# Kernel tuning notes

Measured on AMD Instinct MI355X. Metric: run time of the kernel, lower is better.

The kernel has to match this reference:

```python
import jax, jax.numpy as jnp
import numpy as np

N_NODES = 50000
N_EDGES = 800000
NODE_IN = 5
EDGE_IN = 1
HID = 64


def setup_inputs() -> dict:
    key = jax.random.key(0)
    ks = jax.random.split(key, 16)
    x = jax.random.normal(ks[0], (N_NODES, NODE_IN), dtype=jnp.float32)
    edge_index = jax.random.randint(ks[1], (2, N_EDGES), 0, N_NODES, dtype=jnp.int32)
    edge_attr = jax.random.normal(ks[2], (N_EDGES, EDGE_IN), dtype=jnp.float32)
    def lin(k, fan_in, fan_out):
        b = 1.0 / np.sqrt(fan_in)
        k1, k2 = jax.random.split(k)
        W = jax.random.uniform(k1, (fan_in, fan_out), minval=-b, maxval=b, dtype=jnp.float32)
        bi = jax.random.uniform(k2, (fan_out,), minval=-b, maxval=b, dtype=jnp.float32)
        return W, bi
    W_ne, b_ne = lin(ks[3], NODE_IN, HID)
    W_ee, b_ee = lin(ks[4], EDGE_IN, HID)
    W_gcn, b_gcn = lin(ks[5], HID, HID)   # PyG GCNConv: lin (no bias) + separate bias
    W1, b1 = lin(ks[6], 3 * HID, HID)
    W2, b2 = lin(ks[7], HID, 1)
    return {"x": x, "edge_index": edge_index, "edge_attr": edge_attr,
            "W_ne": W_ne, "b_ne": b_ne, "W_ee": W_ee, "b_ee": b_ee,
            "W_gcn": W_gcn, "b_gcn": b_gcn, "W1": W1, "b1": b1, "W2": W2, "b2": b2}


def gcn_conv(h, edge_index, W, b):
    # PyG GCNConv: add self-loops, symmetric norm D^-1/2 (A+I) D^-1/2, linear, scatter-add.
    N = h.shape[0]
    src, dst = edge_index[0], edge_index[1]
    loops = jnp.arange(N, dtype=src.dtype)
    row = jnp.concatenate([src, loops])  # message sources
    col = jnp.concatenate([dst, loops])  # message targets
    deg = jax.ops.segment_sum(jnp.ones(col.shape[0], h.dtype), col, num_segments=N)
    dinv = jnp.where(deg > 0, jax.lax.rsqrt(deg), 0.0)
    norm = dinv[row] * dinv[col]          # [E+N]
    ht = h @ W                            # [N, HID]
    msg = ht[row] * norm[:, None]         # gather + scale
    return jax.ops.segment_sum(msg, col, num_segments=N) + b


def reference(x, edge_index, edge_attr, W_ne, b_ne, W_ee, b_ee, W_gcn, b_gcn, W1, b1, W2, b2):
    h = jax.nn.relu(x @ W_ne + b_ne)                    # node encoder
    ef = jax.nn.relu(edge_attr @ W_ee + b_ee)           # edge encoder
    h = gcn_conv(h, edge_index, W_gcn, b_gcn)           # GCN layer
    src, dst = edge_index[0], edge_index[1]
    edge_input = jnp.concatenate([h[src], h[dst], ef], axis=1)  # [E, 3*HID]
    out = jax.nn.relu(edge_input @ W1 + b1) @ W2 + b2   # edge MLP -> [E, 1]
    return out.reshape(-1)
```

## Files before the change

kernel.cpp:

```cpp
#include <hip/hip_runtime.h>

#define NN 50000
#define NE 800000
#define H  64
#define NBKT 196
#define BCAP 8192
#define BIN_CHUNK 2048
#define NBIN ((NE + BIN_CHUNK - 1) / BIN_CHUNK)
#define CT4N (65 * 37)
#define ET 5
#define ECHUNK 2

typedef __attribute__((ext_vector_type(8))) short bf16x8;
typedef __attribute__((ext_vector_type(4))) float f32x4;

__device__ __forceinline__ unsigned short f2bf(float f) {
  unsigned int u = __builtin_bit_cast(unsigned int, f);
  u += 0x7FFFu + ((u >> 16) & 1u);
  return (unsigned short)(u >> 16);
}
__device__ __forceinline__ float bf2f(unsigned short u) {
  unsigned int v = ((unsigned int)u) << 16;
  return __builtin_bit_cast(float, v);
}

__global__ __launch_bounds__(256) void k_bin(
    const int* __restrict__ ei, unsigned int* __restrict__ gbin,
    int* __restrict__ gcur,
    const float* __restrict__ W1, const float* __restrict__ b1,
    const float* __restrict__ W_ee, const float* __restrict__ b_ee,
    float* __restrict__ thrS, float* __restrict__ cT,
    unsigned short* __restrict__ w1f) {
  const int t = threadIdx.x;

  if (blockIdx.x == NBIN + 1) {
    const int ln = t & 63, q = t >> 6;
    const int l15_ = ln & 15, l4_ = ln >> 4;
#pragma unroll
    for (int f = 0; f < 4; ++f) {
      const int idx = q * 4 + f;
      const int g = idx >> 3;
      const int ct = (idx >> 1) & 3;
      const int c = idx & 1;
#pragma unroll
      for (int j = 0; j < 8; ++j) {
        const int k = g * 64 + c * 32 + l4_ * 8 + j;
        const int hcol = ct * 16 + l15_;
        w1f[(idx * 64 + ln) * 8 + j] = f2bf(W1[k * H + hcol]);
      }
    }
    return;
  }

  if (blockIdx.x == NBIN) {
    __shared__ float sW1[64][65];
    __shared__ float swee[64], sbee[64], sth[64];
    __shared__ int skx[64];
    for (int i = t; i < 64 * 64; i += 256) {
      const int k = i >> 6, h = i & 63;
      sW1[k][h] = W1[(128 + k) * H + h];
    }
    if (t < 64) {
      const float w = W_ee[t], b = b_ee[t];
      swee[t] = w; sbee[t] = b;
      sth[t] = (w != 0.f) ? (-b / w) : __builtin_inff();
      skx[t] = t;
    }
    __syncthreads();
    for (int sz = 2; sz <= 64; sz <<= 1)
      for (int st = sz >> 1; st > 0; st >>= 1) {
        if (t < 64) {
          const int p = t ^ st;
          if (p > t) {
            const bool up = ((t & sz) == 0);
            const float a = sth[t], bb = sth[p];
            if (up ? (a > bb) : (a < bb)) {
              const int ka = skx[t];
              sth[t] = bb; sth[p] = a;
              skx[t] = skx[p]; skx[p] = ka;
            }
          }
        }
        __syncthreads();
      }
    if (t < 64) {
      const int h = t;
      const int l4h = h >> 4, rh = (h & 15) >> 1, sub = h & 1;
      float c1 = 0.f, c0 = b1[h];
      for (int k = 0; k < 64; ++k) {
        const float w = swee[k], b = sbee[k];
        if (w < 0.f || (w == 0.f && b > 0.f)) {
          const float wv1 = sW1[k][h];
          c1 = fmaf(w, wv1, c1);
          c0 = fmaf(b, wv1, c0);
        }
      }
      {
        float* base = cT + (size_t)(0 * 37 + l4h * 9 + rh) * 4;
        base[2 * sub] = c1; base[2 * sub + 1] = c0;
      }
      for (int iv = 1; iv <= 64; ++iv) {
        const int ks = skx[iv - 1];
        const float w = swee[ks];
        const float s = (w > 0.f) ? 1.f : -1.f;
        const float wv1 = sW1[ks][h];
        c1 = fmaf(s * w, wv1, c1);
        c0 = fmaf(s * sbee[ks], wv1, c0);
        float* base = cT + (size_t)(iv * 37 + l4h * 9 + rh) * 4;
        base[2 * sub] = c1; base[2 * sub + 1] = c0;
      }
      thrS[h] = sth[h];
    }
    return;
  }

  __shared__ int hist[NBKT], base[NBKT];
  if (t < NBKT) hist[t] = 0;
  __syncthreads();

  const int e0 = blockIdx.x * BIN_CHUNK;
  int srcv[8], dstv[8], loff[8];
  if (e0 + BIN_CHUNK <= NE) {
    const int eb = e0 + t * 8;
    const int4 sa = *(const int4*)(ei + eb);
    const int4 sb = *(const int4*)(ei + eb + 4);
    const int4 da = *(const int4*)(ei + NE + eb);
    const int4 db = *(const int4*)(ei + NE + eb + 4);
    srcv[0] = sa.x; srcv[1] = sa.y; srcv[2] = sa.z; srcv[3] = sa.w;
    srcv[4] = sb.x; srcv[5] = sb.y; srcv[6] = sb.z; srcv[7] = sb.w;
    dstv[0] = da.x; dstv[1] = da.y; dstv[2] = da.z; dstv[3] = da.w;
    dstv[4] = db.x; dstv[5] = db.y; dstv[6] = db.z; dstv[7] = db.w;
#pragma unroll
    for (int j = 0; j < 8; ++j) loff[j] = atomicAdd(&hist[dstv[j] >> 8], 1);
  } else {
#pragma unroll
    for (int j = 0; j < 8; ++j) {
      const int e = e0 + t * 8 + j;
      if (e < NE) {
        srcv[j] = ei[e];
        dstv[j] = ei[NE + e];
        loff[j] = atomicAdd(&hist[dstv[j] >> 8], 1);
      } else dstv[j] = -1;
    }
  }
  __syncthreads();
  if (t < NBKT) base[t] = atomicAdd(&gcur[t], hist[t]);
  __syncthreads();
#pragma unroll
  for (int j = 0; j < 8; ++j) {
    if (dstv[j] >= 0) {
      const int b = dstv[j] >> 8;
      const int pos = base[b] + loff[j];
      if (pos < BCAP)
        gbin[(size_t)b * BCAP + pos] =
            ((unsigned int)srcv[j] << 8) | (unsigned int)(dstv[j] & 255);
    }
  }
}

__global__ __launch_bounds__(256) void k_pass2(const unsigned int* __restrict__ gbin,
                                               const int* __restrict__ gcur,
                                               unsigned short* __restrict__ gcsr,
                                               int2* __restrict__ rowrange,
                                               float* __restrict__ dinv) {
  __shared__ int hist[256], cur[256], sc[256];
  __shared__ unsigned short lcsr[BCAP];
  const int b = blockIdx.x, t = threadIdx.x;
  const int sz = min(gcur[b], BCAP);
  hist[t] = 0;
  __syncthreads();

  const unsigned int* bb = gbin + (size_t)b * BCAP;
  unsigned int ent[32];
#pragma unroll
  for (int k = 0; k < 32; ++k) {
    const int i = t + k * 256;
    if (i < sz) {
      ent[k] = bb[i];
      atomicAdd(&hist[ent[k] & 255], 1);
    }
  }
  __syncthreads();

  int v = hist[t];
  const int cnt = v;
  sc[t] = v;
  __syncthreads();
#pragma unroll
  for (int off = 1; off < 256; off <<= 1) {
    const int o = (t >= off) ? sc[t - off] : 0;
    __syncthreads();
    v += o;
    sc[t] = v;
    __syncthreads();
  }
  const int ex = v - cnt;
  cur[t] = ex;
  const int d = b * 256 + t;
  if (d < NN) {
    const int beg = b * BCAP + ex;
    rowrange[d] = make_int2(beg, beg + cnt);
    dinv[d] = rsqrtf((float)(cnt + 1));
  }
  __syncthreads();

#pragma unroll
  for (int k = 0; k < 32; ++k) {
    const int i = t + k * 256;
    if (i < sz) {
      const unsigned int en = ent[k];
      const int off = atomicAdd(&cur[en & 255], 1);
      lcsr[off] = (unsigned short)(en >> 8);
    }
  }
  __syncthreads();
  {
    const int n4 = (sz + 7) >> 3;
    uint4* gdst = (uint4*)(gcsr + (size_t)b * BCAP);
    const uint4* lsrc = (const uint4*)lcsr;
    for (int i = t; i < n4; i += 256) gdst[i] = lsrc[i];
  }
}

__global__ __launch_bounds__(256) void k_node(
    const float* __restrict__ x, const float* __restrict__ W_ne,
    const float* __restrict__ b_ne, const float* __restrict__ W_gcn,
    const float* __restrict__ dinv, unsigned short* __restrict__ htb) {
  __shared__ float sh[4][H];
  const int lane = threadIdx.x & 63;
  const int wv   = threadIdx.x >> 6;
  const int n    = blockIdx.x * 4 + wv;

  float acc = b_ne[lane];
#pragma unroll
  for (int k = 0; k < 5; ++k) acc = fmaf(x[n * 5 + k], W_ne[k * H + lane], acc);
  acc = fmaxf(acc, 0.0f);
  sh[wv][lane] = acc;
  __syncthreads();

  float hv = 0.0f;
#pragma unroll 8
  for (int k = 0; k < H; ++k) hv = fmaf(sh[wv][k], W_gcn[k * H + lane], hv);

  htb[(size_t)n * H + lane] = f2bf(hv * dinv[n]);
}

__global__ __launch_bounds__(256) void k_gather_uv(
    const int2* __restrict__ rowrange, const unsigned short* __restrict__ gcsr,
    const unsigned short* __restrict__ htb, const float* __restrict__ dinv,
    const float* __restrict__ b_gcn, const unsigned short* __restrict__ w1f,
    unsigned short* __restrict__ u, unsigned short* __restrict__ v) {
  __shared__ unsigned short shg[16 * 64];
  const int lane = threadIdx.x & 63;
  const int wv   = threadIdx.x >> 6;
  const int n0   = blockIdx.x * 16;
  const float bg = b_gcn[lane];

#pragma unroll 1
  for (int q = 0; q < 4; ++q) {
    const int nl = wv * 4 + q;
    const int n  = n0 + nl;
    const int2 rr = rowrange[n];
    float sum = bf2f(htb[(size_t)n * H + lane]);
    int i = rr.x;
#pragma unroll 1
    for (; i + 8 <= rr.y; i += 8) {
      const int s0 = gcsr[i],     s1 = gcsr[i + 1];
      const int s2 = gcsr[i + 2], s3 = gcsr[i + 3];
      const int s4 = gcsr[i + 4], s5 = gcsr[i + 5];
      const int s6 = gcsr[i + 6], s7 = gcsr[i + 7];
      const float v0 = bf2f(htb[(size_t)s0 * H + lane]);
      const float v1 = bf2f(htb[(size_t)s1 * H + lane]);
      const float v2 = bf2f(htb[(size_t)s2 * H + lane]);
      const float v3 = bf2f(htb[(size_t)s3 * H + lane]);
      const float v4 = bf2f(htb[(size_t)s4 * H + lane]);
      const float v5 = bf2f(htb[(size_t)s5 * H + lane]);
      const float v6 = bf2f(htb[(size_t)s6 * H + lane]);
      const float v7 = bf2f(htb[(size_t)s7 * H + lane]);
      sum += ((v0 + v1) + (v2 + v3)) + ((v4 + v5) + (v6 + v7));
    }
#pragma unroll 1
    for (; i < rr.y; ++i) sum += bf2f(htb[(size_t)gcsr[i] * H + lane]);

    const float hgv = fmaf(dinv[n], sum, bg);
    shg[((nl * 128 + lane * 2) ^ ((nl & 7) << 4)) >> 1] = f2bf(hgv);
  }
  __syncthreads();

  const int l15 = lane & 15, l4 = lane >> 4;
  const bf16x8 a0 = *(const bf16x8*)(shg + (((l15 * 128 + l4 * 16) ^ ((l15 & 7) << 4)) >> 1));
  const bf16x8 a1 = *(const bf16x8*)(shg + (((l15 * 128 + 64 + l4 * 16) ^ ((l15 & 7) << 4)) >> 1));

  const int ct = wv;
  const bf16x8 bu0 = *(const bf16x8*)(w1f + ((ct * 2 + 0) * 64 + lane) * 8);
  const bf16x8 bu1 = *(const bf16x8*)(w1f + ((ct * 2 + 1) * 64 + lane) * 8);
  const bf16x8 bv0 = *(const bf16x8*)(w1f + ((8 + ct * 2 + 0) * 64 + lane) * 8);
  const bf16x8 bv1 = *(const bf16x8*)(w1f + ((8 + ct * 2 + 1) * 64 + lane) * 8);

  f32x4 au = (f32x4)(0.f), av = (f32x4)(0.f);
  au = __builtin_amdgcn_mfma_f32_16x16x32_bf16(a0, bu0, au, 0, 0, 0);
  au = __builtin_amdgcn_mfma_f32_16x16x32_bf16(a1, bu1, au, 0, 0, 0);
  av = __builtin_amdgcn_mfma_f32_16x16x32_bf16(a0, bv0, av, 0, 0, 0);
  av = __builtin_amdgcn_mfma_f32_16x16x32_bf16(a1, bv1, av, 0, 0, 0);

#pragma unroll
  for (int r = 0; r < 4; ++r) {
    const size_t idx = (size_t)(n0 + l4 * 4 + r) * H + ct * 16 + l15;
    u[idx] = f2bf(au[r]);
    v[idx] = f2bf(av[r]);
  }
}

__device__ __forceinline__ int find_iv(const float* __restrict__ sThr, float ea) {
  int iv = 0;
#pragma unroll
  for (int st = 64; st >= 1; st >>= 1) {
    const int nc = iv + st;
    if (nc <= 64 && sThr[nc - 1] <= ea) iv = nc;
  }
  return iv;
}

__device__ __forceinline__ void edge_compute(
    float ea, uint4 U0, uint4 U1, uint4 V0, uint4 V1,
    const float* __restrict__ sThr, const float4* __restrict__ sCT4,
    const float* __restrict__ w2v, int l4, int lane, float b2v,
    float* __restrict__ out, int obase) {
  const int iv = find_iv(sThr, ea);
  const float4* cp = sCT4 + iv * 37 + l4 * 9;
  const unsigned int ud[8] = {U0.x, U0.y, U0.z, U0.w, U1.x, U1.y, U1.z, U1.w};
  const unsigned int vd[8] = {V0.x, V0.y, V0.z, V0.w, V1.x, V1.y, V1.z, V1.w};
  float p = 0.f;
#pragma unroll
  for (int r = 0; r < 8; ++r) {
    const float4 cc = cp[r];
    const float ulo = __builtin_bit_cast(float, ud[r] << 16);
    const float uhi = __builtin_bit_cast(float, ud[r] & 0xFFFF0000u);
    const float vlo = __builtin_bit_cast(float, vd[r] << 16);
    const float vhi = __builtin_bit_cast(float, vd[r] & 0xFFFF0000u);
    const float z0 = ulo + vlo + fmaf(ea, cc.x, cc.y);
    const float z1 = uhi + vhi + fmaf(ea, cc.z, cc.w);
    p = fmaf(fmaxf(z0, 0.f), w2v[2 * r], p);
    p = fmaf(fmaxf(z1, 0.f), w2v[2 * r + 1], p);
  }
  p += __shfl_xor(p, 16);
  p += __shfl_xor(p, 32);
  if (lane < 16) out[obase + lane] = p + b2v;
}

__global__ __launch_bounds__(512) void k_edge(
    const int* __restrict__ ei, const float* __restrict__ eattr,
    const unsigned short* __restrict__ u, const unsigned short* __restrict__ v,
    const float* __restrict__ thrS, const float* __restrict__ cT,
    const float* __restrict__ W2, const float* __restrict__ b2,
    float* __restrict__ out) {
  __shared__ float sThr[64];
  __shared__ float4 sCT4[CT4N];

  const int t = threadIdx.x;
  if (t < 64) sThr[t] = thrS[t];
  {
    const float4* g = (const float4*)cT;
    for (int i = t; i < CT4N; i += 512) sCT4[i] = g[i];
  }
  __syncthreads();

  const int lane = t & 63;
  const int wv   = t >> 6;
  const int l15  = lane & 15, l4 = lane >> 4;
  const float b2v = b2[0];

  float w2v[16];
#pragma unroll
  for (int j = 0; j < 16; ++j) w2v[j] = W2[l4 * 16 + j];

#pragma unroll 1
  for (int c = 0; c < ECHUNK; ++c) {
    const int tile0 = (((c * 625) + blockIdx.x) * 8 + wv) * ET;
    int srcA[ET], dstA[ET];
    float eaA[ET];
#pragma unroll
    for (int tt = 0; tt < ET; ++tt) {
      srcA[tt] = ei[(tile0 + tt) * 16 + l15];
      dstA[tt] = ei[NE + (tile0 + tt) * 16 + l15];
      eaA[tt]  = eattr[(tile0 + tt) * 16 + l15];
    }

    uint4 Au0, Au1, Av0, Av1, Bu0, Bu1, Bv0, Bv1;

#define LOADUV(U0, U1, V0, V1, tt) {                               \
    const unsigned short* up = u + (size_t)srcA[tt] * H + l4 * 16; \
    const unsigned short* vp = v + (size_t)dstA[tt] * H + l4 * 16; \
    U0 = *(const uint4*)(up); U1 = *(const uint4*)(up + 8);        \
    V0 = *(const uint4*)(vp); V1 = *(const uint4*)(vp + 8); }

    LOADUV(Au0, Au1, Av0, Av1, 0);
    LOADUV(Bu0, Bu1, Bv0, Bv1, 1);
    edge_compute(eaA[0], Au0, Au1, Av0, Av1, sThr, sCT4, w2v, l4, lane, b2v, out, (tile0 + 0) * 16);
    LOADUV(Au0, Au1, Av0, Av1, 2);
    edge_compute(eaA[1], Bu0, Bu1, Bv0, Bv1, sThr, sCT4, w2v, l4, lane, b2v, out, (tile0 + 1) * 16);
    LOADUV(Bu0, Bu1, Bv0, Bv1, 3);
    edge_compute(eaA[2], Au0, Au1, Av0, Av1, sThr, sCT4, w2v, l4, lane, b2v, out, (tile0 + 2) * 16);
    LOADUV(Au0, Au1, Av0, Av1, 4);
    edge_compute(eaA[3], Bu0, Bu1, Bv0, Bv1, sThr, sCT4, w2v, l4, lane, b2v, out, (tile0 + 3) * 16);
    edge_compute(eaA[4], Au0, Au1, Av0, Av1, sThr, sCT4, w2v, l4, lane, b2v, out, (tile0 + 4) * 16);
#undef LOADUV
  }
}

extern "C" void kernel_launch(void* const* d_in, const int* in_sizes, int n_in,
                              void* d_out, int out_size, void* d_ws, size_t ws_size,
                              hipStream_t stream) {
  const float* x     = (const float*)d_in[0];
  const int*   ei    = (const int*)d_in[1];
  const float* eattr = (const float*)d_in[2];
  const float* W_ne  = (const float*)d_in[3];
  const float* b_ne  = (const float*)d_in[4];
  const float* W_ee  = (const float*)d_in[5];
  const float* b_ee  = (const float*)d_in[6];
  const float* W_gcn = (const float*)d_in[7];
  const float* b_gcn = (const float*)d_in[8];
  const float* W1    = (const float*)d_in[9];
  const float* b1    = (const float*)d_in[10];
  const float* W2    = (const float*)d_in[11];
  const float* b2    = (const float*)d_in[12];
  float* out = (float*)d_out;

  char* ws = (char*)d_ws;
  unsigned short* htb = (unsigned short*)(ws + 0);
  unsigned short* uT  = (unsigned short*)(ws + 6400000);
  unsigned int*   gbin = (unsigned int*)(ws + 12800000);
  unsigned short* vT  = (unsigned short*)(ws + 12800000);
  unsigned short* gcsr = (unsigned short*)(ws + 19222528);
  int2*  rowrange = (int2*)(ws + 22433792);
  float* dinv    = (float*)(ws + 22833792);
  int*   gcur    = (int*)(ws + 23033792);
  float* thrS    = (float*)(ws + 23034592);
  float* cT      = (float*)(ws + 23034848);
  unsigned short* w1f = (unsigned short*)(ws + 23073328);

  hipMemsetAsync(gcur, 0, NBKT * sizeof(int), stream);
  k_bin<<<NBIN + 2, 256, 0, stream>>>(ei, gbin, gcur, W1, b1, W_ee, b_ee, thrS, cT, w1f);
  k_pass2<<<NBKT, 256, 0, stream>>>(gbin, gcur, gcsr, rowrange, dinv);
  k_node<<<NN / 4, 256, 0, stream>>>(x, W_ne, b_ne, W_gcn, dinv, htb);
  k_gather_uv<<<NN / 16, 256, 0, stream>>>(rowrange, gcsr, htb, dinv, b_gcn, w1f, uT, vT);
  k_edge<<<625, 512, 0, stream>>>(ei, eattr, uT, vT, thrS, cT, W2, b2, out);
}
```

Measured before the change: 143.4 us.

## Fuse node encoder into CSR pass via global degree counts; shrink edge tiles

```diff
diff --git a/kernel.cpp b/kernel.cpp
--- a/kernel.cpp
+++ b/kernel.cpp
@@ -8,8 +8,7 @@
 #define BIN_CHUNK 2048
 #define NBIN ((NE + BIN_CHUNK - 1) / BIN_CHUNK)
 #define CT4N (65 * 37)
-#define ET 5
-#define ECHUNK 2
+#define ET 2
 
 typedef __attribute__((ext_vector_type(8))) short bf16x8;
 typedef __attribute__((ext_vector_type(4))) float f32x4;
@@ -26,7 +25,7 @@
 
 __global__ __launch_bounds__(256) void k_bin(
     const int* __restrict__ ei, unsigned int* __restrict__ gbin,
-    int* __restrict__ gcur,
+    int* __restrict__ gcur, int* __restrict__ cnt,
     const float* __restrict__ W1, const float* __restrict__ b1,
     const float* __restrict__ W_ee, const float* __restrict__ b_ee,
     float* __restrict__ thrS, float* __restrict__ cT,
@@ -131,7 +130,10 @@
     dstv[0] = da.x; dstv[1] = da.y; dstv[2] = da.z; dstv[3] = da.w;
     dstv[4] = db.x; dstv[5] = db.y; dstv[6] = db.z; dstv[7] = db.w;
 #pragma unroll
-    for (int j = 0; j < 8; ++j) loff[j] = atomicAdd(&hist[dstv[j] >> 8], 1);
+    for (int j = 0; j < 8; ++j) {
+      loff[j] = atomicAdd(&hist[dstv[j] >> 8], 1);
+      atomicAdd(&cnt[dstv[j]], 1);
+    }
   } else {
 #pragma unroll
     for (int j = 0; j < 8; ++j) {
@@ -140,6 +142,7 @@
         srcv[j] = ei[e];
         dstv[j] = ei[NE + e];
         loff[j] = atomicAdd(&hist[dstv[j] >> 8], 1);
+        atomicAdd(&cnt[dstv[j]], 1);
       } else dstv[j] = -1;
     }
   }
@@ -158,14 +161,41 @@
   }
 }
 
-__global__ __launch_bounds__(256) void k_pass2(const unsigned int* __restrict__ gbin,
-                                               const int* __restrict__ gcur,
-                                               unsigned short* __restrict__ gcsr,
-                                               int2* __restrict__ rowrange,
-                                               float* __restrict__ dinv) {
-  __shared__ int hist[256], cur[256], sc[256];
-  __shared__ unsigned short lcsr[BCAP];
-  const int b = blockIdx.x, t = threadIdx.x;
+__global__ __launch_bounds__(256) void k_pn(
+    const unsigned int* __restrict__ gbin, const int* __restrict__ gcur,
+    const int* __restrict__ cnt,
+    unsigned short* __restrict__ gcsr, int2* __restrict__ rowrange,
+    float* __restrict__ dinv,
+    const float* __restrict__ x, const float* __restrict__ W_ne,
+    const float* __restrict__ b_ne, const float* __restrict__ W_gcn,
+    unsigned short* __restrict__ htb) {
+  __shared__ char smem[256 * 12 + BCAP * 2];
+  const int t = threadIdx.x;
+
+  if (blockIdx.x >= NBKT) {
+    float* sh = (float*)smem;
+    const int lane = t & 63;
+    const int wv   = t >> 6;
+    const int n    = (blockIdx.x - NBKT) * 4 + wv;
+    float acc = b_ne[lane];
+#pragma unroll
+    for (int k = 0; k < 5; ++k) acc = fmaf(x[n * 5 + k], W_ne[k * H + lane], acc);
+    acc = fmaxf(acc, 0.0f);
+    sh[wv * H + lane] = acc;
+    __syncthreads();
+    float hv = 0.0f;
+#pragma unroll 8
+    for (int k = 0; k < H; ++k) hv = fmaf(sh[wv * H + k], W_gcn[k * H + lane], hv);
+    const float dv = rsqrtf((float)(cnt[n] + 1));
+    htb[(size_t)n * H + lane] = f2bf(hv * dv);
+    return;
+  }
+
+  int* hist = (int*)smem;
+  int* cur  = hist + 256;
+  int* sc   = cur + 256;
+  unsigned short* lcsr = (unsigned short*)(sc + 256);
+  const int b = blockIdx.x;
   const int sz = min(gcur[b], BCAP);
   hist[t] = 0;
   __syncthreads();
@@ -183,7 +213,7 @@
   __syncthreads();
 
   int v = hist[t];
-  const int cnt = v;
+  const int cv = v;
   sc[t] = v;
   __syncthreads();
 #pragma unroll
@@ -194,13 +224,13 @@
     sc[t] = v;
     __syncthreads();
   }
-  const int ex = v - cnt;
+  const int ex = v - cv;
   cur[t] = ex;
   const int d = b * 256 + t;
   if (d < NN) {
     const int beg = b * BCAP + ex;
-    rowrange[d] = make_int2(beg, beg + cnt);
-    dinv[d] = rsqrtf((float)(cnt + 1));
+    rowrange[d] = make_int2(beg, beg + cv);
+    dinv[d] = rsqrtf((float)(cv + 1));
   }
   __syncthreads();
 
@@ -220,29 +250,6 @@
     const uint4* lsrc = (const uint4*)lcsr;
     for (int i = t; i < n4; i += 256) gdst[i] = lsrc[i];
   }
-}
-
-__global__ __launch_bounds__(256) void k_node(
-    const float* __restrict__ x, const float* __restrict__ W_ne,
-    const float* __restrict__ b_ne, const float* __restrict__ W_gcn,
-    const float* __restrict__ dinv, unsigned short* __restrict__ htb) {
-  __shared__ float sh[4][H];
-  const int lane = threadIdx.x & 63;
-  const int wv   = threadIdx.x >> 6;
-  const int n    = blockIdx.x * 4 + wv;
-
-  float acc = b_ne[lane];
-#pragma unroll
-  for (int k = 0; k < 5; ++k) acc = fmaf(x[n * 5 + k], W_ne[k * H + lane], acc);
-  acc = fmaxf(acc, 0.0f);
-  sh[wv][lane] = acc;
-  __syncthreads();
-
-  float hv = 0.0f;
-#pragma unroll 8
-  for (int k = 0; k < H; ++k) hv = fmaf(sh[wv][k], W_gcn[k * H + lane], hv);
-
-  htb[(size_t)n * H + lane] = f2bf(hv * dinv[n]);
 }
 
 __global__ __launch_bounds__(256) void k_gather_uv(
@@ -374,19 +381,17 @@
 #pragma unroll
   for (int j = 0; j < 16; ++j) w2v[j] = W2[l4 * 16 + j];
 
-#pragma unroll 1
-  for (int c = 0; c < ECHUNK; ++c) {
-    const int tile0 = (((c * 625) + blockIdx.x) * 8 + wv) * ET;
-    int srcA[ET], dstA[ET];
-    float eaA[ET];
-#pragma unroll
-    for (int tt = 0; tt < ET; ++tt) {
-      srcA[tt] = ei[(tile0 + tt) * 16 + l15];
-      dstA[tt] = ei[NE + (tile0 + tt) * 16 + l15];
-      eaA[tt]  = eattr[(tile0 + tt) * 16 + l15];
-    }
-
-    uint4 Au0, Au1, Av0, Av1, Bu0, Bu1, Bv0, Bv1;
+  const int tile0 = (blockIdx.x * 8 + wv) * ET;
+  int srcA[ET], dstA[ET];
+  float eaA[ET];
+#pragma unroll
+  for (int tt = 0; tt < ET; ++tt) {
+    srcA[tt] = ei[(tile0 + tt) * 16 + l15];
+    dstA[tt] = ei[NE + (tile0 + tt) * 16 + l15];
+    eaA[tt]  = eattr[(tile0 + tt) * 16 + l15];
+  }
+
+  uint4 Au0, Au1, Av0, Av1, Bu0, Bu1, Bv0, Bv1;
 
 #define LOADUV(U0, U1, V0, V1, tt) {                               \
     const unsigned short* up = u + (size_t)srcA[tt] * H + l4 * 16; \
@@ -394,18 +399,11 @@
     U0 = *(const uint4*)(up); U1 = *(const uint4*)(up + 8);        \
     V0 = *(const uint4*)(vp); V1 = *(const uint4*)(vp + 8); }
 
-    LOADUV(Au0, Au1, Av0, Av1, 0);
-    LOADUV(Bu0, Bu1, Bv0, Bv1, 1);
-    edge_compute(eaA[0], Au0, Au1, Av0, Av1, sThr, sCT4, w2v, l4, lane, b2v, out, (tile0 + 0) * 16);
-    LOADUV(Au0, Au1, Av0, Av1, 2);
-    edge_compute(eaA[1], Bu0, Bu1, Bv0, Bv1, sThr, sCT4, w2v, l4, lane, b2v, out, (tile0 + 1) * 16);
-    LOADUV(Bu0, Bu1, Bv0, Bv1, 3);
-    edge_compute(eaA[2], Au0, Au1, Av0, Av1, sThr, sCT4, w2v, l4, lane, b2v, out, (tile0 + 2) * 16);
-    LOADUV(Au0, Au1, Av0, Av1, 4);
-    edge_compute(eaA[3], Bu0, Bu1, Bv0, Bv1, sThr, sCT4, w2v, l4, lane, b2v, out, (tile0 + 3) * 16);
-    edge_compute(eaA[4], Au0, Au1, Av0, Av1, sThr, sCT4, w2v, l4, lane, b2v, out, (tile0 + 4) * 16);
+  LOADUV(Au0, Au1, Av0, Av1, 0);
+  LOADUV(Bu0, Bu1, Bv0, Bv1, 1);
+  edge_compute(eaA[0], Au0, Au1, Av0, Av1, sThr, sCT4, w2v, l4, lane, b2v, out, (tile0 + 0) * 16);
+  edge_compute(eaA[1], Bu0, Bu1, Bv0, Bv1, sThr, sCT4, w2v, l4, lane, b2v, out, (tile0 + 1) * 16);
 #undef LOADUV
-  }
 }
 
 extern "C" void kernel_launch(void* const* d_in, const int* in_sizes, int n_in,
@@ -434,15 +432,16 @@
   unsigned short* gcsr = (unsigned short*)(ws + 19222528);
   int2*  rowrange = (int2*)(ws + 22433792);
   float* dinv    = (float*)(ws + 22833792);
-  int*   gcur    = (int*)(ws + 23033792);
-  float* thrS    = (float*)(ws + 23034592);
-  float* cT      = (float*)(ws + 23034848);
-  unsigned short* w1f = (unsigned short*)(ws + 23073328);
-
-  hipMemsetAsync(gcur, 0, NBKT * sizeof(int), stream);
-  k_bin<<<NBIN + 2, 256, 0, stream>>>(ei, gbin, gcur, W1, b1, W_ee, b_ee, thrS, cT, w1f);
-  k_pass2<<<NBKT, 256, 0, stream>>>(gbin, gcur, gcsr, rowrange, dinv);
-  k_node<<<NN / 4, 256, 0, stream>>>(x, W_ne, b_ne, W_gcn, dinv, htb);
+  int*   cnt     = (int*)(ws + 23033792);
+  int*   gcur    = (int*)(ws + 23233792);
+  float* thrS    = (float*)(ws + 23234576);
+  float* cT      = (float*)(ws + 23234832);
+  unsigned short* w1f = (unsigned short*)(ws + 23273312);
+
+  hipMemsetAsync(cnt, 0, 200000 + 784, stream);
+  k_bin<<<NBIN + 2, 256, 0, stream>>>(ei, gbin, gcur, cnt, W1, b1, W_ee, b_ee, thrS, cT, w1f);
+  k_pn<<<NBKT + NN / 4, 256, 0, stream>>>(gbin, gcur, cnt, gcsr, rowrange, dinv,
+                                          x, W_ne, b_ne, W_gcn, htb);
   k_gather_uv<<<NN / 16, 256, 0, stream>>>(rowrange, gcsr, htb, dinv, b_gcn, w1f, uT, vT);
-  k_edge<<<625, 512, 0, stream>>>(ei, eattr, uT, vT, thrS, cT, W2, b2, out);
-}
+  k_edge<<<3125, 512, 0, stream>>>(ei, eattr, uT, vT, thrS, cT, W2, b2, out);
+}
```

Result: slower. 166.6 us (+16.2%).
